# Performance work log

Hardware: AMD Instinct MI355X
Metric: run time of the kernel (lower is better)

## Reference

```python
import jax, jax.numpy as jnp
import numpy as np

B, T, EMB, H1, H2, NL, LMAX, VOCAB = 32, 20, 32, 64, 128, 4, 1024, 85
EPS = 1e-5

def _lengths():
    # ragged per-structure atom counts, max = 1024 (fixes pad length), sum = 24832
    return 1024 - np.arange(B) * 16

def _lstm(x, Wih0, Whh0, b0, WihS, WhhS, bS):
    """NL-layer batch-first LSTM, torch gate order (i,f,g,o), initial h/c = ones
    (matching the torch code's ones init states). Returns stacked final
    (h, c) per layer, each (NL, batch, hidden)."""
    n = x.shape[0]
    hidden = Whh0.shape[1]
    h_fin, c_fin = [], []
    inp = x
    for l in range(NL):
        Wih = Wih0 if l == 0 else WihS[l - 1]
        Whh = Whh0 if l == 0 else WhhS[l - 1]
        bb = b0 if l == 0 else bS[l - 1]
        xg = jnp.einsum('bti,gi->btg', inp, Wih) + bb  # (n, t, 4*hidden)
        init = (jnp.ones((n, hidden), x.dtype), jnp.ones((n, hidden), x.dtype))
        def step(carry, xt, Whh=Whh):
            h, c = carry
            g = xt + h @ Whh.T
            i, f, gg, o = jnp.split(g, 4, axis=-1)
            c = jax.nn.sigmoid(f) * c + jax.nn.sigmoid(i) * jnp.tanh(gg)
            h = jax.nn.sigmoid(o) * jnp.tanh(c)
            return (h, c), h
        (hT, cT), hs = jax.lax.scan(step, init, jnp.swapaxes(xg, 0, 1))
        inp = jnp.swapaxes(hs, 0, 1)
        h_fin.append(hT)
        c_fin.append(cT)
    return jnp.stack(h_fin), jnp.stack(c_fin)

def _bn_rows(x, g, b):
    # BatchNorm1d(batch_size) applied to x.T in torch: per-row (per-structure)
    # normalization over the feature axis, training-mode (biased var).
    m = x.mean(1, keepdims=True)
    v = x.var(1, keepdims=True)
    return (x - m) * jax.lax.rsqrt(v + EPS) * g[:, None] + b[:, None]

def setup_inputs():
    lengths = _lengths()
    N = int(lengths.sum())
    ks = jax.random.split(jax.random.key(0), 32)
    ki = iter(range(32))
    def nrm(shape, s):
        return s * jax.random.normal(ks[next(ki)], shape, jnp.float32)
    return {
        'neighbor_atom_batch': jax.random.randint(ks[next(ki)], (N * T,), 0, VOCAB, dtype=jnp.int32),
        'neighbors_distan_batch': jax.random.normal(ks[next(ki)], (N * T,), jnp.float32),
        'structure_num_bacth': jnp.asarray(lengths, jnp.int32),
        'batch_idx': jnp.asarray(np.repeat(np.arange(B), lengths), jnp.int32),
        'pos_idx': jnp.asarray(np.concatenate([np.arange(l) for l in lengths]), jnp.int32),
        'embed_w': nrm((VOCAB, EMB), 0.02),
        'l1_Wih0': nrm((4 * H1, EMB), 0.05), 'l1_Whh0': nrm((4 * H1, H1), 0.05), 'l1_b0': nrm((4 * H1,), 0.02),
        'l1_Wih': nrm((NL - 1, 4 * H1, H1), 0.05), 'l1_Whh': nrm((NL - 1, 4 * H1, H1), 0.05), 'l1_b': nrm((NL - 1, 4 * H1), 0.02),
        'l2_Wih0': nrm((4 * H2, H1), 0.05), 'l2_Whh0': nrm((4 * H2, H2), 0.05), 'l2_b0': nrm((4 * H2,), 0.02),
        'l2_Wih': nrm((NL - 1, 4 * H2, H2), 0.05), 'l2_Whh': nrm((NL - 1, 4 * H2, H2), 0.05), 'l2_b': nrm((NL - 1, 4 * H2), 0.02),
        'bn2_g': jnp.ones((B,), jnp.float32), 'bn2_b': jnp.zeros((B,), jnp.float32),
        'bn3_g': jnp.ones((B,), jnp.float32), 'bn3_b': jnp.zeros((B,), jnp.float32),
        'w1': nrm((128, 128), 0.1), 'b1': 0.1 * jnp.ones((128,), jnp.float32),
        'w2': nrm((64, 128), 0.1), 'b2': 0.1 * jnp.ones((64,), jnp.float32),
        'w22': nrm((64, 64), 0.1), 'b22': 0.1 * jnp.ones((64,), jnp.float32),
        'w3': nrm((32, 64), 0.1), 'b3': 0.1 * jnp.ones((32,), jnp.float32),
        'w4': nrm((32, 32), 0.1), 'b4': 0.1 * jnp.ones((32,), jnp.float32),
        'w5': nrm((16, 32), 0.1), 'b5': 0.1 * jnp.ones((16,), jnp.float32),
    }

def reference(neighbor_atom_batch, neighbors_distan_batch, structure_num_bacth,
              batch_idx, pos_idx, embed_w,
              l1_Wih0, l1_Whh0, l1_b0, l1_Wih, l1_Whh, l1_b,
              l2_Wih0, l2_Whh0, l2_b0, l2_Wih, l2_Whh, l2_b,
              bn2_g, bn2_b, bn3_g, bn3_b,
              w1, b1, w2, b2, w22, b22, w3, b3, w4, b4, w5, b5):
    # NOTE: neighbors_distan_batch is an argument of the torch forward but is
    # never used by its body; we keep it for signature fidelity.
    # embed, then scale each embedding row by its own integer atom id (as torch does)
    x = embed_w[neighbor_atom_batch] * neighbor_atom_batch.astype(jnp.float32)[:, None]
    x = x.reshape(-1, T, EMB)                       # (N, 20, 32)
    hT, cT = _lstm(x, l1_Wih0, l1_Whh0, l1_b0, l1_Wih, l1_Whh, l1_b)
    d = hT.mean(0) + cT.mean(0)                     # (N, 64)
    # ragged split by structure_num_bacth + pad_sequence -> (B, LMAX, 64), zero padded
    padded = jnp.zeros((B, LMAX, H1), d.dtype).at[batch_idx, pos_idx].set(d)
    # BatchNorm1d(batch_size): channel dim is the structure index -> stats over (len, feat)
    m = padded.mean((1, 2), keepdims=True)
    v = padded.var((1, 2), keepdims=True)
    padded = (padded - m) * jax.lax.rsqrt(v + EPS) * bn2_g[:, None, None] + bn2_b[:, None, None]
    _, cT2 = _lstm(padded, l2_Wih0, l2_Whh0, l2_b0, l2_Wih, l2_Whh, l2_b)
    d = cT2.mean(0)                                 # (B, 128) mean of final cell states
    d = _bn_rows(d, bn3_g, bn3_b)
    d = jax.nn.relu(d @ w1.T + b1)
    d = jax.nn.relu(d @ w2.T + b2)
    d = _bn_rows(d, bn3_g, bn3_b)                   # same BN layer reused, as in torch
    d = jax.nn.relu(d @ w22.T + b22)
    d = jax.nn.relu(d @ w3.T + b3)
    d = jax.nn.relu(d @ w4.T + b4)
    d = d @ w5.T + b5                               # (B, 16)
    return jax.nn.relu(d.sum(1))                    # (B,)
```

## Files before the change

kernel.cpp:

```cpp
#include <hip/hip_runtime.h>


typedef _Float16 f16x8  __attribute__((ext_vector_type(8)));
typedef float    f32x4  __attribute__((ext_vector_type(4)));

#define DEVI static __device__ __forceinline__

constexpr int   T1c   = 20;
constexpr int   EMBc  = 32;
constexpr int   H1c   = 64;
constexpr int   LMAXc = 1024;
constexpr int   VOCABc= 85;
constexpr int   Ntot  = 24832;
constexpr int   NTc   = Ntot * T1c;
constexpr int   R2c   = 32 * LMAXc;
constexpr float EPSc  = 1e-5f;

DEVI float sigm(float x)   { return 1.f / (1.f + __expf(-x)); }
DEVI float tanhf_(float x) { return 1.f - 2.f / (1.f + __expf(2.f * x)); }

DEVI void barrier_lds() {
    asm volatile("s_waitcnt lgkmcnt(0)\n\ts_barrier" ::: "memory");
}
DEVI void drain_vmem() {
    asm volatile("s_waitcnt vmcnt(0)" ::: "memory");
}

__global__ void __launch_bounds__(256)
k_prepw1(const float* __restrict__ Wih0, const float* __restrict__ Whh0,
         const float* __restrict__ WihS, const float* __restrict__ WhhS,
         _Float16* __restrict__ out)
{
    int i = blockIdx.x * 256 + threadIdx.x;
    if (i >= 4 * 256 * 128) return;
    int l = i >> 15, rem = i & 32767, r = rem >> 7, k = rem & 127;
    float v;
    if (l == 0) {
        if (k < 32)      v = Wih0[r * 32 + k];
        else if (k < 64) v = 0.f;
        else             v = Whh0[r * 64 + (k - 64)];
    } else {
        if (k < 64)      v = WihS[((l - 1) * 256 + r) * 64 + k];
        else             v = WhhS[((l - 1) * 256 + r) * 64 + (k - 64)];
    }
    out[i] = (_Float16)v;
}

__global__ void __launch_bounds__(256)
k_prepw2(const float* __restrict__ Wih0, const float* __restrict__ WihS,
         const float* __restrict__ Whh0, const float* __restrict__ WhhS,
         _Float16* __restrict__ wih, _Float16* __restrict__ whh,
         int* __restrict__ flags)
{
    int i = blockIdx.x * 256 + threadIdx.x;
    if (i < 512) flags[i] = (i < 256) ? 0 : 0x7fffffff;
    if (i >= 2 * 4 * 512 * 128) return;
    int half = i >> 18, rem = i & 262143;
    int l = rem >> 16, r = (rem >> 7) & 511, k = rem & 127;
    if (half == 0) {
        float v = (l == 0) ? ((k < 64) ? Wih0[r * 64 + k] : 0.f)
                           : WihS[((l - 1) * 512 + r) * 128 + k];
        wih[rem] = (_Float16)v;
    } else {
        float v = (l == 0) ? Whh0[r * 128 + k]
                           : WhhS[((l - 1) * 512 + r) * 128 + k];
        whh[rem] = (_Float16)v;
    }
}

__global__ void __launch_bounds__(256)
k_scan1all(const int* __restrict__ atoms, const float* __restrict__ ew,
           const _Float16* __restrict__ W16all,
           const float* __restrict__ b0, const float* __restrict__ bS,
           _Float16* __restrict__ seq, float* __restrict__ dacc)
{
    constexpr int SX = 136;
    __shared__ alignas(16) _Float16 xh[32 * SX];
    __shared__ float ewl[VOCABc * EMBc];
    __shared__ int   aidl[32 * T1c];

    const int tid  = threadIdx.x;
    const int lane = tid & 63;
    const int wv   = tid >> 6;
    const int l16  = lane & 15;
    const int quad = lane >> 4;
    const int n0   = blockIdx.x * 32;
    const int d    = wv * 16 + l16;

    for (int i = tid; i < VOCABc * EMBc; i += 256) ewl[i] = ew[i];
    for (int i = tid; i < 32 * T1c; i += 256) aidl[i] = atoms[n0 * T1c + i];

    float daccv[2][4];
#pragma unroll
    for (int mt = 0; mt < 2; ++mt)
#pragma unroll
        for (int r = 0; r < 4; ++r) daccv[mt][r] = 0.f;

    __syncthreads();

#pragma unroll 1
    for (int l = 0; l < 4; ++l) {
        const _Float16* W16  = W16all + (size_t)l * 256 * 128;
        const float*    bptr = (l == 0) ? b0 : bS + (l - 1) * 256;

        float bias[4];
#pragma unroll
        for (int g = 0; g < 4; ++g) bias[g] = bptr[g * 64 + d];

        f16x8 wF[4][4];
#pragma unroll
        for (int kc = 0; kc < 4; ++kc) {
            const int kb = kc * 32 + quad * 8;
#pragma unroll
            for (int g = 0; g < 4; ++g)
                wF[kc][g] = *(const f16x8*)&W16[(size_t)(g * 64 + d) * 128 + kb];
        }

        f32x4 c[2];
        c[0] = {1.f, 1.f, 1.f, 1.f};
        c[1] = {1.f, 1.f, 1.f, 1.f};

        drain_vmem();
        __syncthreads();

#pragma unroll
        for (int mt = 0; mt < 2; ++mt)
#pragma unroll
            for (int r = 0; r < 4; ++r)
                xh[(mt * 16 + quad * 4 + r) * SX + 64 + d] = (_Float16)1.0f;
        if (l == 0)
            for (int idx = tid; idx < 32 * 32; idx += 256) {
                int s = idx >> 5, e = idx & 31;
                xh[s * SX + 32 + e] = (_Float16)0.f;
            }

#pragma unroll 1
        for (int t = 0; t < T1c; ++t) {
            if (l == 0) {
                for (int idx = tid; idx < 32 * 32; idx += 256) {
                    int s = idx >> 5, e = idx & 31;
                    int id = aidl[s * T1c + t];
                    xh[s * SX + e] = (_Float16)(ewl[id * EMBc + e] * (float)id);
                }
            } else {
                for (int idx = tid; idx < 32 * 8; idx += 256) {
                    int s = idx >> 3, k8 = idx & 7;
                    *(f16x8*)&xh[s * SX + k8 * 8] =
                        *(const f16x8*)&seq[((size_t)(n0 + s) * T1c + t) * H1c + k8 * 8];
                }
            }
            __syncthreads();

            f32x4 acc[2][4];
#pragma unroll
            for (int mt = 0; mt < 2; ++mt)
#pragma unroll
                for (int g = 0; g < 4; ++g)
                    acc[mt][g] = {bias[g], bias[g], bias[g], bias[g]};

#pragma unroll
            for (int kc = 0; kc < 4; ++kc) {
                const int kb = kc * 32 + quad * 8;
                f16x8 ah[2];
#pragma unroll
                for (int mt = 0; mt < 2; ++mt)
                    ah[mt] = *(const f16x8*)&xh[(mt * 16 + l16) * SX + kb];
#pragma unroll
                for (int g = 0; g < 4; ++g)
#pragma unroll
                    for (int mt = 0; mt < 2; ++mt)
                        acc[mt][g] = __builtin_amdgcn_mfma_f32_16x16x32_f16(ah[mt], wF[kc][g], acc[mt][g], 0, 0, 0);
            }
            __syncthreads();

#pragma unroll
            for (int mt = 0; mt < 2; ++mt)
#pragma unroll
                for (int r = 0; r < 4; ++r) {
                    float iv = sigm(acc[mt][0][r]);
                    float fv = sigm(acc[mt][1][r]);
                    float gv = tanhf_(acc[mt][2][r]);
                    float ov = sigm(acc[mt][3][r]);
                    float cv = fv * c[mt][r] + iv * gv;
                    c[mt][r] = cv;
                    float hv = ov * tanhf_(cv);
                    _Float16 hf = (_Float16)hv;
                    int s = mt * 16 + quad * 4 + r;
                    xh[s * SX + 64 + d] = hf;
                    if (l < 3)
                        seq[((size_t)(n0 + s) * T1c + t) * H1c + d] = hf;
                    if (t == T1c - 1)
                        daccv[mt][r] += 0.25f * (hv + cv);
                }
        }
    }
#pragma unroll
    for (int mt = 0; mt < 2; ++mt)
#pragma unroll
        for (int r = 0; r < 4; ++r) {
            int s = mt * 16 + quad * 4 + r;
            dacc[(size_t)(n0 + s) * H1c + d] = daccv[mt][r];
        }
}

__global__ void __launch_bounds__(256)
k_bn2_stats(const int* __restrict__ lens, const float* __restrict__ dacc,
            float* __restrict__ stats)
{
    int b = blockIdx.x;
    int off = 0;
    for (int i = 0; i < b; ++i) off += lens[i];
    int len = lens[b];
    const float* base = dacc + (long)off * H1c;
    float s = 0.f, ss = 0.f;
    int total = len * H1c;
    for (int i = threadIdx.x; i < total; i += 256) { float v = base[i]; s += v; ss += v * v; }
    __shared__ float rs[256], rss[256];
    rs[threadIdx.x] = s; rss[threadIdx.x] = ss;
    __syncthreads();
    for (int st = 128; st > 0; st >>= 1) {
        if (threadIdx.x < st) { rs[threadIdx.x] += rs[threadIdx.x + st]; rss[threadIdx.x] += rss[threadIdx.x + st]; }
        __syncthreads();
    }
    if (threadIdx.x == 0) {
        float m = rs[0] / (float)(LMAXc * H1c);
        float v = rss[0] / (float)(LMAXc * H1c) - m * m;
        stats[b]      = m;
        stats[32 + b] = rsqrtf(fmaxf(v, 0.f) + EPSc);
        stats[64 + b] = (float)off;
    }
}

__global__ void __launch_bounds__(256)
k_bn2_apply(const float* __restrict__ dacc, const float* __restrict__ stats,
            const int* __restrict__ lens, const float* __restrict__ g,
            const float* __restrict__ bb, _Float16* __restrict__ outA)
{
    int i = blockIdx.x * 256 + threadIdx.x;
    if (i >= R2c * 128) return;
    int rr = i >> 7, k = i & 127;
    int b = rr >> 10, p = rr & 1023;
    float y = 0.f;
    if (k < H1c) {
        int off = (int)stats[64 + b];
        float x = (p < lens[b]) ? dacc[(off + p) * H1c + k] : 0.f;
        y = (x - stats[b]) * stats[32 + b] * g[b] + bb[b];
    }
    outA[(size_t)(p * 32 + b) * 128 + k] = (_Float16)y;
}

DEVI float qsel(f32x4 a, int quad) {
    float t01 = (quad & 1) ? a[1] : a[0];
    float t23 = (quad & 1) ? a[3] : a[2];
    return (quad & 2) ? t23 : t01;
}

DEVI void spin_ge(const int* fl, int lane, int need)
{
    for (;;) {
        int f = 0x7fffffff;
        if (lane < 8)
            asm volatile("global_load_dword %0, %1, off sc0 sc1\n\ts_waitcnt vmcnt(0)"
                         : "+v"(f) : "v"(fl) : "memory");
        if (__all(f >= need)) break;
    }
}

#define STEP(T, PAR, R, F)                                                          \
  {                                                                                 \
    f32x4 accX[4], accH[4];                                                         \
    _Pragma("unroll") for (int g4 = 0; g4 < 4; ++g4) {                              \
        accX[g4] = {bia[g4], bia[g4], bia[g4], bia[g4]};                            \
        accH[g4] = {0.f, 0.f, 0.f, 0.f};                                            \
    }                                                                               \
    _Pragma("unroll") for (int kc = 0; kc < 4; ++kc) {                              \
        f16x8 ax = *(const f16x8*)&xp[PAR][(l16 & 3) * SH + kc * 32 + quad * 8];    \
        _Pragma("unroll") for (int g4 = 0; g4 < 4; ++g4)                            \
            accX[g4] = __builtin_amdgcn_mfma_f32_16x16x32_f16(ax, wI[g4][kc], accX[g4], 0, 0, 0); \
    }                                                                               \
    _Pragma("unroll") for (int kc = 0; kc < 4; ++kc) {                              \
        f16x8 ah = *(const f16x8*)&av[PAR][(l16 & 3) * SH + kc * 32 + quad * 8];    \
        _Pragma("unroll") for (int g4 = 0; g4 < 4; ++g4)                            \
            accH[g4] = __builtin_amdgcn_mfma_f32_16x16x32_f16(ah, wH[g4][kc], accH[g4], 0, 0, 0); \
    }                                                                               \
    asm volatile("s_waitcnt vmcnt(4)" ::: "memory");                                \
    __builtin_amdgcn_sched_barrier(0);                                              \
    if (lane == 0) {                                                                \
        int fv = (T) - 1;                                                           \
        asm volatile("global_store_dword %0, %1, off sc0 sc1"                       \
                     :: "v"(myflag), "v"(fv) : "memory");                           \
    }                                                                               \
    *(unsigned*)&xp[PAR ^ 1][csam * SH + 2 * coff] = R;                             \
    float gi = qsel(accX[0], quad) + qsel(accH[0], quad);                           \
    float gf = qsel(accX[1], quad) + qsel(accH[1], quad);                           \
    float gg = qsel(accX[2], quad) + qsel(accH[2], quad);                           \
    float go = qsel(accX[3], quad) + qsel(accH[3], quad);                           \
    float cv = sigm(gf) * cst + sigm(gi) * tanhf_(gg);                              \
    cst = cv;                                                                       \
    float hv = sigm(go) * tanhf_(cv);                                               \
    _Float16 hf = (_Float16)hv;                                                     \
    av[PAR ^ 1][quad * SH + cell] = hf;                                             \
    {                                                                               \
        int need = ((T) <= LMAXc - 4) ? (T) + 4 : 0;                                \
        if (!__all(lane >= 8 || F >= need)) spin_ge(sflag, lane, need);             \
    }                                                                               \
    if (l == 0)                                                                     \
        asm volatile("global_load_dword %0, %1, off" : "=v"(R) : "v"(xq) : "memory"); \
    else                                                                            \
        asm volatile("global_load_dword %0, %1, off sc0 sc1" : "=v"(R) : "v"(xq) : "memory"); \
    if ((T) < LMAXc - 4) xq += xstep;                                               \
    {   unsigned hb = (unsigned)__builtin_bit_cast(unsigned short, hf);             \
        asm volatile("global_store_short %0, %1, off sc0 sc1"                       \
                     :: "v"(hp), "v"(hb) : "memory"); }                             \
    hp += 512;                                                                      \
    if (lane < 8)                                                                   \
        asm volatile("global_load_dword %0, %1, off sc0 sc1"                        \
                     : "+v"(F) : "v"(sflag) : "memory");                            \
    barrier_lds();                                                                  \
  }

__global__ void
__attribute__((amdgpu_flat_work_group_size(512, 512), amdgpu_waves_per_eu(2, 2)))
k_scan2p(const _Float16* __restrict__ seqA,
         const _Float16* __restrict__ wihAll,
         const _Float16* __restrict__ whhAll,
         const float* __restrict__ b0,
         const float* __restrict__ bS,
         _Float16* __restrict__ hbuf,
         int* __restrict__ flags,
         float* __restrict__ c2)
{
    constexpr int SH = 144;
    __shared__ alignas(16) _Float16 av[2][4 * SH];
    __shared__ alignas(16) _Float16 xp[2][4 * SH];

    const int bx   = blockIdx.x;
    const int l    = bx & 3;
    const int g    = bx >> 2;
    const int tid  = threadIdx.x;
    const int lane = tid & 63;
    const int w    = tid >> 6;
    const int l16  = lane & 15;
    const int quad = lane >> 4;
    const int cell = w * 16 + l16;

    const _Float16* Wih = wihAll + (size_t)l * 512 * 128;
    const _Float16* Whh = whhAll + (size_t)l * 512 * 128;
    const float*   bptr = (l == 0) ? b0 : bS + (l - 1) * 512;

    f16x8 wI[4][4], wH[4][4];
    float bia[4];
#pragma unroll
    for (int g4 = 0; g4 < 4; ++g4) {
#pragma unroll
        for (int kc = 0; kc < 4; ++kc) {
            const _Float16* pI = &Wih[(size_t)(g4 * 128 + cell) * 128 + kc * 32 + quad * 8];
            const _Float16* pH = &Whh[(size_t)(g4 * 128 + cell) * 128 + kc * 32 + quad * 8];
            asm volatile("global_load_dwordx4 %0, %1, off" : "=v"(wI[g4][kc]) : "v"(pI));
            asm volatile("global_load_dwordx4 %0, %1, off" : "=v"(wH[g4][kc]) : "v"(pH));
        }
        const float* pb = &bptr[g4 * 128 + cell];
        asm volatile("global_load_dword %0, %1, off" : "=v"(bia[g4]) : "v"(pb));
    }
    drain_vmem();
    __builtin_amdgcn_sched_barrier(0);

    const int ci   = tid & 255;
    const int csam = ci >> 6;
    const int coff = ci & 63;

    const unsigned* xq;
    int xstep;
    if (l == 0) {
        xq    = (const unsigned*)seqA + ((size_t)(g * 4 + csam)) * 64 + coff;
        xstep = 32 * 64;
    } else {
        xq    = (const unsigned*)(hbuf + ((size_t)((l - 1) * 8 + g)) * (LMAXc * 512)) + ci;
        xstep = 256;
    }

    _Float16*  hp     = hbuf + ((size_t)(l * 8 + g)) * (LMAXc * 512) + quad * 128 + cell;
    int*       myflag = flags + (l * 8 + g) * 8 + w;
    const int* sflag  = (l == 0) ? (flags + 256 + (lane & 7))
                                 : (flags + ((l - 1) * 8 + g) * 8 + (lane & 7));

    { int s = tid >> 7, e = tid & 127; av[0][s * SH + e] = (_Float16)1.0f; }
    float cst = 1.f;

    unsigned rA, rB;
    int fpreA = 0, fpreB = 0;

    spin_ge(sflag, lane, 1);
    if (l == 0) asm volatile("global_load_dword %0, %1, off" : "=v"(rA) : "v"(xq) : "memory");
    else        asm volatile("global_load_dword %0, %1, off sc0 sc1" : "=v"(rA) : "v"(xq) : "memory");
    drain_vmem();
    __builtin_amdgcn_sched_barrier(0);
    *(unsigned*)&xp[0][csam * SH + 2 * coff] = rA;

    spin_ge(sflag, lane, 2);
    {
        const unsigned* p1 = xq + xstep;
        if (l == 0) asm volatile("global_load_dword %0, %1, off" : "=v"(rA) : "v"(p1) : "memory");
        else        asm volatile("global_load_dword %0, %1, off sc0 sc1" : "=v"(rA) : "v"(p1) : "memory");
    }
    drain_vmem();
    __builtin_amdgcn_sched_barrier(0);

    spin_ge(sflag, lane, 3);
    {
        const unsigned* p2 = xq + 2 * xstep;
        if (l == 0) asm volatile("global_load_dword %0, %1, off" : "=v"(rB) : "v"(p2) : "memory");
        else        asm volatile("global_load_dword %0, %1, off sc0 sc1" : "=v"(rB) : "v"(p2) : "memory");
    }
    if (lane < 8) {
        asm volatile("global_load_dword %0, %1, off sc0 sc1" : "+v"(fpreA) : "v"(sflag) : "memory");
        asm volatile("global_load_dword %0, %1, off sc0 sc1" : "+v"(fpreB) : "v"(sflag) : "memory");
    }
    xq += 3 * (size_t)xstep;
    __syncthreads();

#pragma unroll 1
    for (int t = 0; t < LMAXc; t += 2) {
        STEP(t,     0, rA, fpreA)
        STEP(t + 1, 1, rB, fpreB)
    }

    drain_vmem();
    if (lane == 0) {
        int fin = LMAXc;
        asm volatile("global_store_dword %0, %1, off sc0 sc1"
                     :: "v"(myflag), "v"(fin) : "memory");
    }
    c2[(size_t)l * 4096 + (g * 4 + quad) * 128 + cell] = 0.25f * cst;
}

DEVI void bn_rows_dev(float* X, int K, const float* g, const float* bb,
                      float* mv, int tid)
{
    __syncthreads();
    if (tid < 32) {
        float s = 0.f, ss = 0.f;
        const float* r = X + tid * K;
        for (int k = 0; k < K; ++k) { float v = r[k]; s += v; ss += v * v; }
        float m = s / (float)K;
        float vv = ss / (float)K - m * m;
        mv[tid]      = m;
        mv[32 + tid] = rsqrtf(fmaxf(vv, 0.f) + EPSc);
    }
    __syncthreads();
    for (int i = tid; i < 32 * K; i += 256) {
        int b = i / K;
        X[i] = (X[i] - mv[b]) * mv[32 + b] * g[b] + bb[b];
    }
    __syncthreads();
}

DEVI void lin_dev(const float* X, int K, const float* W, const float* bias,
                  int NO, float* Y, int relu, int tid)
{
    __syncthreads();
    for (int i = tid; i < 32 * NO; i += 256) {
        int b = i / NO, j = i - b * NO;
        float a = bias[j];
        const float* xr = X + b * K;
        const float* wr = W + j * K;
        for (int k = 0; k < K; ++k) a += xr[k] * wr[k];
        Y[i] = relu ? fmaxf(a, 0.f) : a;
    }
    __syncthreads();
}

__global__ void __launch_bounds__(256)
k_head(const float* __restrict__ c2, const float* __restrict__ g3, const float* __restrict__ bb3,
       const float* w1, const float* b1, const float* w2, const float* b2,
       const float* w22, const float* b22, const float* w3, const float* b3,
       const float* w4, const float* b4, const float* w5, const float* b5,
       float* __restrict__ out)
{
    __shared__ float A[32 * 128];
    __shared__ float Bf[32 * 128];
    __shared__ float mv[64];
    const int tid = threadIdx.x;

    for (int i = tid; i < 32 * 128; i += 256)
        A[i] = c2[i] + c2[4096 + i] + c2[8192 + i] + c2[12288 + i];
    bn_rows_dev(A, 128, g3, bb3, mv, tid);
    lin_dev(A, 128, w1, b1, 128, Bf, 1, tid);
    lin_dev(Bf, 128, w2, b2, 64, A, 1, tid);
    bn_rows_dev(A, 64, g3, bb3, mv, tid);
    lin_dev(A, 64, w22, b22, 64, Bf, 1, tid);
    lin_dev(Bf, 64, w3, b3, 32, A, 1, tid);
    lin_dev(A, 32, w4, b4, 32, Bf, 1, tid);
    lin_dev(Bf, 32, w5, b5, 16, A, 0, tid);
    if (tid < 32) {
        float s = 0.f;
        for (int j = 0; j < 16; ++j) s += A[tid * 16 + j];
        out[tid] = fmaxf(s, 0.f);
    }
}

extern "C" void kernel_launch(void* const* d_in, const int* in_sizes, int n_in,
                              void* d_out, int out_size, void* d_ws, size_t ws_size,
                              hipStream_t stream)
{
    const int*   atoms  = (const int*)d_in[0];
    const int*   lens   = (const int*)d_in[2];
    const float* embw   = (const float*)d_in[5];
    const float* l1Wih0 = (const float*)d_in[6];
    const float* l1Whh0 = (const float*)d_in[7];
    const float* l1b0   = (const float*)d_in[8];
    const float* l1Wih  = (const float*)d_in[9];
    const float* l1Whh  = (const float*)d_in[10];
    const float* l1b    = (const float*)d_in[11];
    const float* l2Wih0 = (const float*)d_in[12];
    const float* l2Whh0 = (const float*)d_in[13];
    const float* l2b0   = (const float*)d_in[14];
    const float* l2Wih  = (const float*)d_in[15];
    const float* l2Whh  = (const float*)d_in[16];
    const float* l2b    = (const float*)d_in[17];
    const float* bn2g   = (const float*)d_in[18];
    const float* bn2b   = (const float*)d_in[19];
    const float* bn3g   = (const float*)d_in[20];
    const float* bn3b   = (const float*)d_in[21];
    const float* w1  = (const float*)d_in[22]; const float* b1  = (const float*)d_in[23];
    const float* w2  = (const float*)d_in[24]; const float* b2  = (const float*)d_in[25];
    const float* w22 = (const float*)d_in[26]; const float* b22 = (const float*)d_in[27];
    const float* w3  = (const float*)d_in[28]; const float* b3  = (const float*)d_in[29];
    const float* w4  = (const float*)d_in[30]; const float* b4  = (const float*)d_in[31];
    const float* w5  = (const float*)d_in[32]; const float* b5  = (const float*)d_in[33];
    float* out = (float*)d_out;

    char* base = (char*)d_ws;
    size_t off = 0;
    auto take = [&](size_t bytes) -> char* {
        char* p = base + off;
        off = (off + bytes + 255) & ~(size_t)255;
        return p;
    };
    _Float16* seq1f  = (_Float16*)take((size_t)NTc * H1c * 2);
    float*    dacc   = (float*)take((size_t)Ntot * H1c * 4);
    _Float16* wcomb1 = (_Float16*)take((size_t)4 * 256 * 128 * 2);
    _Float16* wih16  = (_Float16*)take((size_t)4 * 512 * 128 * 2);
    _Float16* whh16  = (_Float16*)take((size_t)4 * 512 * 128 * 2);
    _Float16* seqA   = (_Float16*)take((size_t)R2c * 128 * 2);
    _Float16* hbuf   = (_Float16*)take((size_t)4 * 8 * LMAXc * 512 * 2);
    int*      flags  = (int*)take(512 * sizeof(int));
    float*    stats  = (float*)take(1024);
    float*    c2     = (float*)take((size_t)4 * 32 * 128 * 4);

    k_prepw1<<<(4 * 256 * 128 + 255) / 256, 256, 0, stream>>>(l1Wih0, l1Whh0, l1Wih, l1Whh, wcomb1);
    k_prepw2<<<(2 * 4 * 512 * 128 + 255) / 256, 256, 0, stream>>>(l2Wih0, l2Wih, l2Whh0, l2Whh, wih16, whh16, flags);

    k_scan1all<<<Ntot / 32, 256, 0, stream>>>(atoms, embw, wcomb1, l1b0, l1b, seq1f, dacc);

    k_bn2_stats<<<32, 256, 0, stream>>>(lens, dacc, stats);
    k_bn2_apply<<<(R2c * 128 + 255) / 256, 256, 0, stream>>>(dacc, stats, lens, bn2g, bn2b, seqA);

    k_scan2p<<<32, 512, 0, stream>>>(seqA, wih16, whh16, l2b0, l2b, hbuf, flags, c2);

    k_head<<<1, 256, 0, stream>>>(c2, bn3g, bn3b, w1, b1, w2, b2, w22, b22,
                                  w3, b3, w4, b4, w5, b5, out);

    (void)in_sizes; (void)n_in; (void)out_size; (void)ws_size;
}
```

Measured before the change: 1.746 ms.

## Split LSTM2 into recurrent and input-projection workgroups with a ring buffer

The second LSTM scan kernel now launches twice as many workgroups. Half compute only the recurrent h·Whh product per step. The other half precompute the input projection x·Wih plus bias four timesteps at a time and hand the gate pre-activations over through a 64-slot ring buffer in global memory, synchronised with flags. Weights move from registers into LDS. The aim is to shorten the serial per-step critical path by taking the input GEMM off it, at the cost of extra global traffic, spin-waits on flags, and more complex cross-block synchronisation.

Result: slower. 2.743 ms (+57.2%).

```diff
diff --git a/kernel.cpp b/kernel.cpp
--- a/kernel.cpp
+++ b/kernel.cpp
@@ -2,9 +2,11 @@
 
 
 typedef _Float16 f16x8  __attribute__((ext_vector_type(8)));
+typedef _Float16 f16x4  __attribute__((ext_vector_type(4)));
 typedef float    f32x4  __attribute__((ext_vector_type(4)));
 
 #define DEVI static __device__ __forceinline__
+#define MF(a, b, c) __builtin_amdgcn_mfma_f32_16x16x32_f16(a, b, c, 0, 0, 0)
 
 constexpr int   T1c   = 20;
 constexpr int   EMBc  = 32;
@@ -15,6 +17,7 @@
 constexpr int   NTc   = Ntot * T1c;
 constexpr int   R2c   = 32 * LMAXc;
 constexpr float EPSc  = 1e-5f;
+constexpr int   SH    = 144;
 
 DEVI float sigm(float x)   { return 1.f / (1.f + __expf(-x)); }
 DEVI float tanhf_(float x) { return 1.f - 2.f / (1.f + __expf(2.f * x)); }
@@ -53,7 +56,7 @@
          int* __restrict__ flags)
 {
     int i = blockIdx.x * 256 + threadIdx.x;
-    if (i < 512) flags[i] = (i < 256) ? 0 : 0x7fffffff;
+    if (i < 768) flags[i] = (i < 512) ? 0 : 0x7fffffff;
     if (i >= 2 * 4 * 512 * 128) return;
     int half = i >> 18, rem = i & 262143;
     int l = rem >> 16, r = (rem >> 7) & 511, k = rem & 127;
@@ -169,7 +172,7 @@
                 for (int g = 0; g < 4; ++g)
 #pragma unroll
                     for (int mt = 0; mt < 2; ++mt)
-                        acc[mt][g] = __builtin_amdgcn_mfma_f32_16x16x32_f16(ah[mt], wF[kc][g], acc[mt][g], 0, 0, 0);
+                        acc[mt][g] = MF(ah[mt], wF[kc][g], acc[mt][g]);
             }
             __syncthreads();
 
@@ -266,49 +269,42 @@
     }
 }
 
-#define STEP(T, PAR, R, F)                                                          \
+#define STEPH(T, PAR, RU, F)                                                        \
   {                                                                                 \
-    f32x4 accX[4], accH[4];                                                         \
-    _Pragma("unroll") for (int g4 = 0; g4 < 4; ++g4) {                              \
-        accX[g4] = {bia[g4], bia[g4], bia[g4], bia[g4]};                            \
-        accH[g4] = {0.f, 0.f, 0.f, 0.f};                                            \
-    }                                                                               \
-    _Pragma("unroll") for (int kc = 0; kc < 4; ++kc) {                              \
-        f16x8 ax = *(const f16x8*)&xp[PAR][(l16 & 3) * SH + kc * 32 + quad * 8];    \
-        _Pragma("unroll") for (int g4 = 0; g4 < 4; ++g4)                            \
-            accX[g4] = __builtin_amdgcn_mfma_f32_16x16x32_f16(ax, wI[g4][kc], accX[g4], 0, 0, 0); \
-    }                                                                               \
+    f32x4 a0 = {0,0,0,0}, a1 = {0,0,0,0}, a2 = {0,0,0,0}, a3 = {0,0,0,0};           \
     _Pragma("unroll") for (int kc = 0; kc < 4; ++kc) {                              \
         f16x8 ah = *(const f16x8*)&av[PAR][(l16 & 3) * SH + kc * 32 + quad * 8];    \
-        _Pragma("unroll") for (int g4 = 0; g4 < 4; ++g4)                            \
-            accH[g4] = __builtin_amdgcn_mfma_f32_16x16x32_f16(ah, wH[g4][kc], accH[g4], 0, 0, 0); \
-    }                                                                               \
-    asm volatile("s_waitcnt vmcnt(4)" ::: "memory");                                \
+        a0 = MF(ah, *(const f16x8*)&wL[(0 * 4 + kc) * 4096 + wbase], a0);           \
+        a1 = MF(ah, *(const f16x8*)&wL[(1 * 4 + kc) * 4096 + wbase], a1);           \
+        a2 = MF(ah, *(const f16x8*)&wL[(2 * 4 + kc) * 4096 + wbase], a2);           \
+        a3 = MF(ah, *(const f16x8*)&wL[(3 * 4 + kc) * 4096 + wbase], a3);           \
+    }                                                                               \
+    asm volatile("s_waitcnt vmcnt(28)" ::: "memory");                               \
     __builtin_amdgcn_sched_barrier(0);                                              \
     if (lane == 0) {                                                                \
-        int fv = (T) - 1;                                                           \
+        int fv = (T) >= 7 ? (T) - 7 : 0;                                            \
         asm volatile("global_store_dword %0, %1, off sc0 sc1"                       \
                      :: "v"(myflag), "v"(fv) : "memory");                           \
     }                                                                               \
-    *(unsigned*)&xp[PAR ^ 1][csam * SH + 2 * coff] = R;                             \
-    float gi = qsel(accX[0], quad) + qsel(accH[0], quad);                           \
-    float gf = qsel(accX[1], quad) + qsel(accH[1], quad);                           \
-    float gg = qsel(accX[2], quad) + qsel(accH[2], quad);                           \
-    float go = qsel(accX[3], quad) + qsel(accH[3], quad);                           \
+    float gi = qsel(a0, quad) + (float)RU[0];                                       \
+    float gf = qsel(a1, quad) + (float)RU[1];                                       \
+    float gg = qsel(a2, quad) + (float)RU[2];                                       \
+    float go = qsel(a3, quad) + (float)RU[3];                                       \
     float cv = sigm(gf) * cst + sigm(gi) * tanhf_(gg);                              \
     cst = cv;                                                                       \
     float hv = sigm(go) * tanhf_(cv);                                               \
     _Float16 hf = (_Float16)hv;                                                     \
     av[PAR ^ 1][quad * SH + cell] = hf;                                             \
     {                                                                               \
-        int need = ((T) <= LMAXc - 4) ? (T) + 4 : 0;                                \
+        int need = ((T) + 9 <= LMAXc) ? (T) + 9 : LMAXc;                            \
         if (!__all(lane >= 8 || F >= need)) spin_ge(sflag, lane, need);             \
     }                                                                               \
-    if (l == 0)                                                                     \
-        asm volatile("global_load_dword %0, %1, off" : "=v"(R) : "v"(xq) : "memory"); \
-    else                                                                            \
-        asm volatile("global_load_dword %0, %1, off sc0 sc1" : "=v"(R) : "v"(xq) : "memory"); \
-    if ((T) < LMAXc - 4) xq += xstep;                                               \
+    {                                                                               \
+        int tu = (T) + 8; if (tu > LMAXc - 1) tu = LMAXc - 1;                       \
+        const _Float16* up = ubase + (size_t)(((tu & 63) * 4 + quad) * 128 + cell) * 4; \
+        asm volatile("global_load_dwordx2 %0, %1, off sc0 sc1"                      \
+                     : "=v"(RU) : "v"(up) : "memory");                              \
+    }                                                                               \
     {   unsigned hb = (unsigned)__builtin_bit_cast(unsigned short, hf);             \
         asm volatile("global_store_short %0, %1, off sc0 sc1"                       \
                      :: "v"(hp), "v"(hb) : "memory"); }                             \
@@ -319,6 +315,67 @@
     barrier_lds();                                                                  \
   }
 
+#define XLOADW(R, P)                                                                \
+    if (l == 0) asm volatile("global_load_dword %0, %1, off" : "=v"(R) : "v"(P) : "memory"); \
+    else        asm volatile("global_load_dword %0, %1, off sc0 sc1" : "=v"(R) : "v"(P) : "memory");
+
+#define ITERW(J, PARX, RA, RB, FA, FT)                                              \
+  {                                                                                 \
+    f32x4 bb = *(const f32x4*)&bL2[cell * 4];                                       \
+    f32x4 a0 = {bb[0],bb[0],bb[0],bb[0]}, a1 = {bb[1],bb[1],bb[1],bb[1]};           \
+    f32x4 a2 = {bb[2],bb[2],bb[2],bb[2]}, a3 = {bb[3],bb[3],bb[3],bb[3]};           \
+    _Pragma("unroll") for (int kc = 0; kc < 4; ++kc) {                              \
+        f16x8 ax = *(const f16x8*)&xp4[PARX][l16 * SH + kc * 32 + quad * 8];        \
+        a0 = MF(ax, *(const f16x8*)&wL[(0 * 4 + kc) * 4096 + wbase], a0);           \
+        a1 = MF(ax, *(const f16x8*)&wL[(1 * 4 + kc) * 4096 + wbase], a1);           \
+        a2 = MF(ax, *(const f16x8*)&wL[(2 * 4 + kc) * 4096 + wbase], a2);           \
+        a3 = MF(ax, *(const f16x8*)&wL[(3 * 4 + kc) * 4096 + wbase], a3);           \
+    }                                                                               \
+    asm volatile("s_waitcnt vmcnt(27)" ::: "memory");                               \
+    __builtin_amdgcn_sched_barrier(0);                                              \
+    if (lane == 0) {                                                                \
+        int fv = 4 * (J) - 12; if (fv < 0) fv = 0;                                  \
+        asm volatile("global_store_dword %0, %1, off sc0 sc1"                       \
+                     :: "v"(myflag), "v"(fv) : "memory");                           \
+    }                                                                               \
+    *(unsigned*)&xp4[PARX ^ 1][rowA * SH + 2 * dcol] = RA;                          \
+    *(unsigned*)&xp4[PARX ^ 1][rowB * SH + 2 * dcol] = RB;                          \
+    {                                                                               \
+        int nt = 4 * (J) - 52; if (nt < 0) nt = 0;                                  \
+        if (!__all(lane >= 8 || FT >= nt)) spin_ge(sflagT, lane, nt);               \
+    }                                                                               \
+    {                                                                               \
+        int slot = (4 * (J) + quad) & 63;                                           \
+        _Pragma("unroll") for (int r = 0; r < 4; ++r) {                             \
+            f16x4 uv;                                                               \
+            uv[0] = (_Float16)a0[r]; uv[1] = (_Float16)a1[r];                       \
+            uv[2] = (_Float16)a2[r]; uv[3] = (_Float16)a3[r];                       \
+            _Float16* up = ubase + (size_t)((slot * 4 + r) * 128 + cell) * 4;       \
+            asm volatile("global_store_dwordx2 %0, %1, off sc0 sc1"                 \
+                         :: "v"(up), "v"(uv) : "memory");                           \
+        }                                                                           \
+    }                                                                               \
+    {                                                                               \
+        int na = 4 * (J) + 24; if (na > LMAXc) na = LMAXc;                          \
+        if (!__all(lane >= 8 || FA >= na)) spin_ge(sflagA, lane, na);               \
+    }                                                                               \
+    {                                                                               \
+        int ta = 4 * (J) + 20 + jA; if (ta > LMAXc - 1) ta = LMAXc - 1;             \
+        int tb = 4 * (J) + 20 + jB; if (tb > LMAXc - 1) tb = LMAXc - 1;             \
+        const unsigned* pa = xb + (size_t)ta * xstepw + baseA;                      \
+        const unsigned* pb = xb + (size_t)tb * xstepw + baseB;                      \
+        XLOADW(RA, pa)                                                              \
+        XLOADW(RB, pb)                                                              \
+    }                                                                               \
+    if (lane < 8) {                                                                 \
+        asm volatile("global_load_dword %0, %1, off sc0 sc1"                        \
+                     : "+v"(FA) : "v"(sflagA) : "memory");                          \
+        asm volatile("global_load_dword %0, %1, off sc0 sc1"                        \
+                     : "+v"(FT) : "v"(sflagT) : "memory");                          \
+    }                                                                               \
+    barrier_lds();                                                                  \
+  }
+
 __global__ void
 __attribute__((amdgpu_flat_work_group_size(512, 512), amdgpu_waves_per_eu(2, 2)))
 k_scan2p(const _Float16* __restrict__ seqA,
@@ -327,111 +384,165 @@
          const float* __restrict__ b0,
          const float* __restrict__ bS,
          _Float16* __restrict__ hbuf,
+         _Float16* __restrict__ ubuf,
          int* __restrict__ flags,
          float* __restrict__ c2)
 {
-    constexpr int SH = 144;
-    __shared__ alignas(16) _Float16 av[2][4 * SH];
-    __shared__ alignas(16) _Float16 xp[2][4 * SH];
+    __shared__ alignas(16) char smem[131072 + 11776];
+    _Float16* wL = (_Float16*)smem;
 
     const int bx   = blockIdx.x;
-    const int l    = bx & 3;
-    const int g    = bx >> 2;
     const int tid  = threadIdx.x;
     const int lane = tid & 63;
     const int w    = tid >> 6;
     const int l16  = lane & 15;
     const int quad = lane >> 4;
     const int cell = w * 16 + l16;
-
-    const _Float16* Wih = wihAll + (size_t)l * 512 * 128;
-    const _Float16* Whh = whhAll + (size_t)l * 512 * 128;
-    const float*   bptr = (l == 0) ? b0 : bS + (l - 1) * 512;
-
-    f16x8 wI[4][4], wH[4][4];
-    float bia[4];
-#pragma unroll
-    for (int g4 = 0; g4 < 4; ++g4) {
-#pragma unroll
-        for (int kc = 0; kc < 4; ++kc) {
-            const _Float16* pI = &Wih[(size_t)(g4 * 128 + cell) * 128 + kc * 32 + quad * 8];
-            const _Float16* pH = &Whh[(size_t)(g4 * 128 + cell) * 128 + kc * 32 + quad * 8];
-            asm volatile("global_load_dwordx4 %0, %1, off" : "=v"(wI[g4][kc]) : "v"(pI));
-            asm volatile("global_load_dwordx4 %0, %1, off" : "=v"(wH[g4][kc]) : "v"(pH));
-        }
-        const float* pb = &bptr[g4 * 128 + cell];
-        asm volatile("global_load_dword %0, %1, off" : "=v"(bia[g4]) : "v"(pb));
-    }
-    drain_vmem();
-    __builtin_amdgcn_sched_barrier(0);
-
-    const int ci   = tid & 255;
-    const int csam = ci >> 6;
-    const int coff = ci & 63;
-
-    const unsigned* xq;
-    int xstep;
-    if (l == 0) {
-        xq    = (const unsigned*)seqA + ((size_t)(g * 4 + csam)) * 64 + coff;
-        xstep = 32 * 64;
+    const int wbase = (w * 64 + lane) * 8;
+
+    if (bx < 32) {
+        const int l = bx & 3, g = bx >> 2;
+        const _Float16* W = whhAll + (size_t)l * 512 * 128;
+        _Float16* avm = (_Float16*)(smem + 131072);
+        _Float16* const av[2] = { avm, avm + 4 * SH };
+
+        for (int c = tid; c < 8192; c += 512) {
+            int gk = c >> 9, r2 = c & 511;
+            int wv2 = r2 >> 6, ln = r2 & 63;
+            int row = (gk >> 2) * 128 + wv2 * 16 + (ln & 15);
+            *(f16x8*)&wL[(size_t)c * 8] =
+                *(const f16x8*)&W[(size_t)row * 128 + (gk & 3) * 32 + (ln >> 4) * 8];
+        }
+        av[0][quad * SH + cell] = (_Float16)1.0f;
+        float cst = 1.f;
+
+        const _Float16* ubase = ubuf + (size_t)(l * 8 + g) * (64 * 4 * 512);
+        _Float16*  hp     = hbuf + (size_t)(l * 8 + g) * (LMAXc * 512) + quad * 128 + cell;
+        int*       myflag = flags + (l * 8 + g) * 8 + w;
+        const int* sflag  = flags + 256 + (l * 8 + g) * 8 + (lane & 7);
+
+        __syncthreads();
+        spin_ge(sflag, lane, 8);
+        f16x4 rU0, rU1, rU2, rU3, rU4, rU5, rU6, rU7;
+#define ULOADP(R, I)                                                                \
+        { const _Float16* up = ubase + (size_t)(((I) * 4 + quad) * 128 + cell) * 4; \
+          asm volatile("global_load_dwordx2 %0, %1, off sc0 sc1"                    \
+                       : "=v"(R) : "v"(up) : "memory"); }
+        ULOADP(rU0, 0) ULOADP(rU1, 1) ULOADP(rU2, 2) ULOADP(rU3, 3)
+        ULOADP(rU4, 4) ULOADP(rU5, 5) ULOADP(rU6, 6) ULOADP(rU7, 7)
+#undef ULOADP
+        int fpreA = 0, fpreB = 0;
+        if (lane < 8) {
+            asm volatile("global_load_dword %0, %1, off sc0 sc1" : "+v"(fpreA) : "v"(sflag) : "memory");
+            asm volatile("global_load_dword %0, %1, off sc0 sc1" : "+v"(fpreB) : "v"(sflag) : "memory");
+        }
+        drain_vmem();
+        __builtin_amdgcn_sched_barrier(0);
+        __syncthreads();
+
+#pragma unroll 1
+        for (int t = 0; t < LMAXc; t += 8) {
+            STEPH(t + 0, 0, rU0, fpreA)
+            STEPH(t + 1, 1, rU1, fpreB)
+            STEPH(t + 2, 0, rU2, fpreA)
+            STEPH(t + 3, 1, rU3, fpreB)
+            STEPH(t + 4, 0, rU4, fpreA)
+            STEPH(t + 5, 1, rU5, fpreB)
+            STEPH(t + 6, 0, rU6, fpreA)
+            STEPH(t + 7, 1, rU7, fpreB)
+        }
+
+        drain_vmem();
+        if (lane == 0) {
+            int fin = 2048;
+            asm volatile("global_store_dword %0, %1, off sc0 sc1"
+                         :: "v"(myflag), "v"(fin) : "memory");
+        }
+        c2[(size_t)l * 4096 + (g * 4 + quad) * 128 + cell] = 0.25f * cst;
     } else {
-        xq    = (const unsigned*)(hbuf + ((size_t)((l - 1) * 8 + g)) * (LMAXc * 512)) + ci;
-        xstep = 256;
-    }
-
-    _Float16*  hp     = hbuf + ((size_t)(l * 8 + g)) * (LMAXc * 512) + quad * 128 + cell;
-    int*       myflag = flags + (l * 8 + g) * 8 + w;
-    const int* sflag  = (l == 0) ? (flags + 256 + (lane & 7))
-                                 : (flags + ((l - 1) * 8 + g) * 8 + (lane & 7));
-
-    { int s = tid >> 7, e = tid & 127; av[0][s * SH + e] = (_Float16)1.0f; }
-    float cst = 1.f;
-
-    unsigned rA, rB;
-    int fpreA = 0, fpreB = 0;
-
-    spin_ge(sflag, lane, 1);
-    if (l == 0) asm volatile("global_load_dword %0, %1, off" : "=v"(rA) : "v"(xq) : "memory");
-    else        asm volatile("global_load_dword %0, %1, off sc0 sc1" : "=v"(rA) : "v"(xq) : "memory");
-    drain_vmem();
-    __builtin_amdgcn_sched_barrier(0);
-    *(unsigned*)&xp[0][csam * SH + 2 * coff] = rA;
-
-    spin_ge(sflag, lane, 2);
-    {
-        const unsigned* p1 = xq + xstep;
-        if (l == 0) asm volatile("global_load_dword %0, %1, off" : "=v"(rA) : "v"(p1) : "memory");
-        else        asm volatile("global_load_dword %0, %1, off sc0 sc1" : "=v"(rA) : "v"(p1) : "memory");
-    }
-    drain_vmem();
-    __builtin_amdgcn_sched_barrier(0);
-
-    spin_ge(sflag, lane, 3);
-    {
-        const unsigned* p2 = xq + 2 * xstep;
-        if (l == 0) asm volatile("global_load_dword %0, %1, off" : "=v"(rB) : "v"(p2) : "memory");
-        else        asm volatile("global_load_dword %0, %1, off sc0 sc1" : "=v"(rB) : "v"(p2) : "memory");
-    }
-    if (lane < 8) {
-        asm volatile("global_load_dword %0, %1, off sc0 sc1" : "+v"(fpreA) : "v"(sflag) : "memory");
-        asm volatile("global_load_dword %0, %1, off sc0 sc1" : "+v"(fpreB) : "v"(sflag) : "memory");
-    }
-    xq += 3 * (size_t)xstep;
-    __syncthreads();
+        const int l = (bx - 32) & 3, g = (bx - 32) >> 2;
+        const _Float16* W = wihAll + (size_t)l * 512 * 128;
+        const float* bptr = (l == 0) ? b0 : bS + (l - 1) * 512;
+        _Float16* xpm = (_Float16*)(smem + 131072);
+        _Float16* const xp4[2] = { xpm, xpm + 16 * SH };
+        float* bL2 = (float*)(smem + 131072 + 9216);
+
+        for (int c = tid; c < 8192; c += 512) {
+            int gk = c >> 9, r2 = c & 511;
+            int wv2 = r2 >> 6, ln = r2 & 63;
+            int row = (gk >> 2) * 128 + wv2 * 16 + (ln & 15);
+            *(f16x8*)&wL[(size_t)c * 8] =
+                *(const f16x8*)&W[(size_t)row * 128 + (gk & 3) * 32 + (ln >> 4) * 8];
+        }
+        bL2[(tid & 127) * 4 + (tid >> 7)] = bptr[(tid >> 7) * 128 + (tid & 127)];
+
+        _Float16*  ubase  = ubuf + (size_t)(l * 8 + g) * (64 * 4 * 512);
+        int*       myflag = flags + 256 + (l * 8 + g) * 8 + w;
+        const int* sflagA = (l == 0) ? flags + 512 + (lane & 7)
+                                     : flags + ((l - 1) * 8 + g) * 8 + (lane & 7);
+        const int* sflagT = flags + (l * 8 + g) * 8 + (lane & 7);
+
+        const int dcol = tid & 63;
+        const int rowA = tid >> 6, rowB = 8 + rowA;
+        const int sA = rowA & 3, jA = rowA >> 2;
+        const int sB = rowB & 3, jB = rowB >> 2;
+        const unsigned* xb;
+        int xstepw, baseA, baseB;
+        if (l == 0) {
+            xb = (const unsigned*)seqA;
+            xstepw = 2048;
+            baseA = (g * 4 + sA) * 64 + dcol;
+            baseB = (g * 4 + sB) * 64 + dcol;
+        } else {
+            xb = (const unsigned*)(hbuf + (size_t)((l - 1) * 8 + g) * (LMAXc * 512));
+            xstepw = 256;
+            baseA = sA * 64 + dcol;
+            baseB = sB * 64 + dcol;
+        }
+
+        __syncthreads();
+        spin_ge(sflagA, lane, 20);
+        unsigned rxa0, rxb0, rxa1, rxb1, rxa2, rxb2, rxa3, rxb3;
+        {
+            unsigned r0, r1;
+            const unsigned* pa = xb + (size_t)jA * xstepw + baseA;
+            const unsigned* pb = xb + (size_t)jB * xstepw + baseB;
+            XLOADW(r0, pa) XLOADW(r1, pb)
+            drain_vmem();
+            __builtin_amdgcn_sched_barrier(0);
+            *(unsigned*)&xp4[0][rowA * SH + 2 * dcol] = r0;
+            *(unsigned*)&xp4[0][rowB * SH + 2 * dcol] = r1;
+        }
+#define XPRE(RA, RB, P)                                                             \
+        { const unsigned* pa = xb + (size_t)(4 * ((P) + 1) + jA) * xstepw + baseA;  \
+          const unsigned* pb = xb + (size_t)(4 * ((P) + 1) + jB) * xstepw + baseB;  \
+          XLOADW(RA, pa) XLOADW(RB, pb) }
+        XPRE(rxa0, rxb0, 0) XPRE(rxa1, rxb1, 1) XPRE(rxa2, rxb2, 2) XPRE(rxa3, rxb3, 3)
+#undef XPRE
+        int fA = 0, fT = 0;
+        if (lane < 8) {
+            asm volatile("global_load_dword %0, %1, off sc0 sc1" : "+v"(fA) : "v"(sflagA) : "memory");
+            asm volatile("global_load_dword %0, %1, off sc0 sc1" : "+v"(fT) : "v"(sflagT) : "memory");
+        }
+        drain_vmem();
+        __builtin_amdgcn_sched_barrier(0);
+        __syncthreads();
 
 #pragma unroll 1
-    for (int t = 0; t < LMAXc; t += 2) {
-        STEP(t,     0, rA, fpreA)
-        STEP(t + 1, 1, rB, fpreB)
-    }
-
-    drain_vmem();
-    if (lane == 0) {
-        int fin = LMAXc;
-        asm volatile("global_store_dword %0, %1, off sc0 sc1"
-                     :: "v"(myflag), "v"(fin) : "memory");
-    }
-    c2[(size_t)l * 4096 + (g * 4 + quad) * 128 + cell] = 0.25f * cst;
+        for (int j = 0; j < 64; ++j) {
+            ITERW(4 * j + 0, 0, rxa0, rxb0, fA, fT)
+            ITERW(4 * j + 1, 1, rxa1, rxb1, fA, fT)
+            ITERW(4 * j + 2, 0, rxa2, rxb2, fA, fT)
+            ITERW(4 * j + 3, 1, rxa3, rxb3, fA, fT)
+        }
+
+        drain_vmem();
+        if (lane == 0) {
+            int fin = 2048;
+            asm volatile("global_store_dword %0, %1, off sc0 sc1"
+                         :: "v"(myflag), "v"(fin) : "memory");
+        }
+    }
 }
 
 DEVI void bn_rows_dev(float* X, int K, const float* g, const float* bb,
@@ -544,7 +655,8 @@
     _Float16* whh16  = (_Float16*)take((size_t)4 * 512 * 128 * 2);
     _Float16* seqA   = (_Float16*)take((size_t)R2c * 128 * 2);
     _Float16* hbuf   = (_Float16*)take((size_t)4 * 8 * LMAXc * 512 * 2);
-    int*      flags  = (int*)take(512 * sizeof(int));
+    _Float16* ubuf   = (_Float16*)take((size_t)4 * 8 * 64 * 4 * 512 * 2);
+    int*      flags  = (int*)take(768 * sizeof(int));
     float*    stats  = (float*)take(1024);
     float*    c2     = (float*)take((size_t)4 * 32 * 128 * 4);
 
@@ -556,7 +668,7 @@
     k_bn2_stats<<<32, 256, 0, stream>>>(lens, dacc, stats);
     k_bn2_apply<<<(R2c * 128 + 255) / 256, 256, 0, stream>>>(dacc, stats, lens, bn2g, bn2b, seqA);
 
-    k_scan2p<<<32, 512, 0, stream>>>(seqA, wih16, whh16, l2b0, l2b, hbuf, flags, c2);
+    k_scan2p<<<64, 512, 0, stream>>>(seqA, wih16, whh16, l2b0, l2b, hbuf, ubuf, flags, c2);
 
     k_head<<<1, 256, 0, stream>>>(c2, bn3g, bn3b, w1, b1, w2, b2, w22, b22,
                                   w3, b3, w4, b4, w5, b5, out);
```

## Keep layer-1 LSTM inter-layer sequence in LDS instead of global memory

Applied to the files above, without the earlier changes.

The first LSTM stack now keeps each layer's hidden-state sequence for a 32-atom tile in shared memory, so the next layer reads it from LDS rather than writing it to and re-reading it from a global workspace. The single combined input/hidden tile becomes a separate embedding tile plus a double-buffered hidden-state tile, which drops one of the barriers around the recurrent state. The goal is to remove global memory traffic and load latency on the recurrence critical path. The cost is about 120 KB of LDS per block, which sharply limits how many blocks can sit on a CU at once and reduces latency hiding for this latency-bound recurrent kernel.

Result: slower. 1.833 ms (+5.0%).

```diff
diff --git a/kernel.cpp b/kernel.cpp
--- a/kernel.cpp
+++ b/kernel.cpp
@@ -5,6 +5,7 @@
 typedef float    f32x4  __attribute__((ext_vector_type(4)));
 
 #define DEVI static __device__ __forceinline__
+#define MF(a, b, c) __builtin_amdgcn_mfma_f32_16x16x32_f16(a, b, c, 0, 0, 0)
 
 constexpr int   T1c   = 20;
 constexpr int   EMBc  = 32;
@@ -12,7 +13,6 @@
 constexpr int   LMAXc = 1024;
 constexpr int   VOCABc= 85;
 constexpr int   Ntot  = 24832;
-constexpr int   NTc   = Ntot * T1c;
 constexpr int   R2c   = 32 * LMAXc;
 constexpr float EPSc  = 1e-5f;
 
@@ -72,10 +72,11 @@
 k_scan1all(const int* __restrict__ atoms, const float* __restrict__ ew,
            const _Float16* __restrict__ W16all,
            const float* __restrict__ b0, const float* __restrict__ bS,
-           _Float16* __restrict__ seq, float* __restrict__ dacc)
-{
-    constexpr int SX = 136;
-    __shared__ alignas(16) _Float16 xh[32 * SX];
+           float* __restrict__ dacc)
+{
+    __shared__ alignas(16) _Float16 seqL[T1c * 32 * 72];
+    __shared__ alignas(16) _Float16 xe[32 * 72];
+    __shared__ alignas(16) _Float16 hP[2][32 * 72];
     __shared__ float ewl[VOCABc * EMBc];
     __shared__ int   aidl[32 * T1c];
 
@@ -89,6 +90,7 @@
 
     for (int i = tid; i < VOCABc * EMBc; i += 256) ewl[i] = ew[i];
     for (int i = tid; i < 32 * T1c; i += 256) aidl[i] = atoms[n0 * T1c + i];
+    for (int i = tid; i < 32 * 72; i += 256) xe[i] = (_Float16)0.f;
 
     float daccv[2][4];
 #pragma unroll
@@ -120,19 +122,16 @@
         c[0] = {1.f, 1.f, 1.f, 1.f};
         c[1] = {1.f, 1.f, 1.f, 1.f};
 
-        drain_vmem();
         __syncthreads();
 
 #pragma unroll
         for (int mt = 0; mt < 2; ++mt)
 #pragma unroll
             for (int r = 0; r < 4; ++r)
-                xh[(mt * 16 + quad * 4 + r) * SX + 64 + d] = (_Float16)1.0f;
-        if (l == 0)
-            for (int idx = tid; idx < 32 * 32; idx += 256) {
-                int s = idx >> 5, e = idx & 31;
-                xh[s * SX + 32 + e] = (_Float16)0.f;
-            }
+                hP[0][(mt * 16 + quad * 4 + r) * 72 + d] = (_Float16)1.0f;
+
+        int par = 0;
+        __syncthreads();
 
 #pragma unroll 1
         for (int t = 0; t < T1c; ++t) {
@@ -140,13 +139,7 @@
                 for (int idx = tid; idx < 32 * 32; idx += 256) {
                     int s = idx >> 5, e = idx & 31;
                     int id = aidl[s * T1c + t];
-                    xh[s * SX + e] = (_Float16)(ewl[id * EMBc + e] * (float)id);
-                }
-            } else {
-                for (int idx = tid; idx < 32 * 8; idx += 256) {
-                    int s = idx >> 3, k8 = idx & 7;
-                    *(f16x8*)&xh[s * SX + k8 * 8] =
-                        *(const f16x8*)&seq[((size_t)(n0 + s) * T1c + t) * H1c + k8 * 8];
+                    xe[s * 72 + e] = (_Float16)(ewl[id * EMBc + e] * (float)id);
                 }
             }
             __syncthreads();
@@ -160,16 +153,24 @@
 
 #pragma unroll
             for (int kc = 0; kc < 4; ++kc) {
-                const int kb = kc * 32 + quad * 8;
                 f16x8 ah[2];
 #pragma unroll
-                for (int mt = 0; mt < 2; ++mt)
-                    ah[mt] = *(const f16x8*)&xh[(mt * 16 + l16) * SX + kb];
+                for (int mt = 0; mt < 2; ++mt) {
+                    const int row = mt * 16 + l16;
+                    const _Float16* src;
+                    if (kc < 2)
+                        src = (l == 0)
+                            ? &xe[row * 72 + kc * 32 + quad * 8]
+                            : &seqL[(t * 32 + row) * 72 + kc * 32 + quad * 8];
+                    else
+                        src = &hP[par][row * 72 + (kc - 2) * 32 + quad * 8];
+                    ah[mt] = *(const f16x8*)src;
+                }
 #pragma unroll
                 for (int g = 0; g < 4; ++g)
 #pragma unroll
                     for (int mt = 0; mt < 2; ++mt)
-                        acc[mt][g] = __builtin_amdgcn_mfma_f32_16x16x32_f16(ah[mt], wF[kc][g], acc[mt][g], 0, 0, 0);
+                        acc[mt][g] = MF(ah[mt], wF[kc][g], acc[mt][g]);
             }
             __syncthreads();
 
@@ -186,12 +187,13 @@
                     float hv = ov * tanhf_(cv);
                     _Float16 hf = (_Float16)hv;
                     int s = mt * 16 + quad * 4 + r;
-                    xh[s * SX + 64 + d] = hf;
+                    hP[par ^ 1][s * 72 + d] = hf;
                     if (l < 3)
-                        seq[((size_t)(n0 + s) * T1c + t) * H1c + d] = hf;
+                        seqL[(t * 32 + s) * 72 + d] = hf;
                     if (t == T1c - 1)
                         daccv[mt][r] += 0.25f * (hv + cv);
                 }
+            par ^= 1;
         }
     }
 #pragma unroll
@@ -276,12 +278,12 @@
     _Pragma("unroll") for (int kc = 0; kc < 4; ++kc) {                              \
         f16x8 ax = *(const f16x8*)&xp[PAR][(l16 & 3) * SH + kc * 32 + quad * 8];    \
         _Pragma("unroll") for (int g4 = 0; g4 < 4; ++g4)                            \
-            accX[g4] = __builtin_amdgcn_mfma_f32_16x16x32_f16(ax, wI[g4][kc], accX[g4], 0, 0, 0); \
+            accX[g4] = MF(ax, wI[g4][kc], accX[g4]);                                \
     }                                                                               \
     _Pragma("unroll") for (int kc = 0; kc < 4; ++kc) {                              \
         f16x8 ah = *(const f16x8*)&av[PAR][(l16 & 3) * SH + kc * 32 + quad * 8];    \
         _Pragma("unroll") for (int g4 = 0; g4 < 4; ++g4)                            \
-            accH[g4] = __builtin_amdgcn_mfma_f32_16x16x32_f16(ah, wH[g4][kc], accH[g4], 0, 0, 0); \
+            accH[g4] = MF(ah, wH[g4][kc], accH[g4]);                                \
     }                                                                               \
     asm volatile("s_waitcnt vmcnt(4)" ::: "memory");                                \
     __builtin_amdgcn_sched_barrier(0);                                              \
@@ -537,7 +539,6 @@
         off = (off + bytes + 255) & ~(size_t)255;
         return p;
     };
-    _Float16* seq1f  = (_Float16*)take((size_t)NTc * H1c * 2);
     float*    dacc   = (float*)take((size_t)Ntot * H1c * 4);
     _Float16* wcomb1 = (_Float16*)take((size_t)4 * 256 * 128 * 2);
     _Float16* wih16  = (_Float16*)take((size_t)4 * 512 * 128 * 2);
@@ -551,7 +552,7 @@
     k_prepw1<<<(4 * 256 * 128 + 255) / 256, 256, 0, stream>>>(l1Wih0, l1Whh0, l1Wih, l1Whh, wcomb1);
     k_prepw2<<<(2 * 4 * 512 * 128 + 255) / 256, 256, 0, stream>>>(l2Wih0, l2Wih, l2Whh0, l2Whh, wih16, whh16, flags);
 
-    k_scan1all<<<Ntot / 32, 256, 0, stream>>>(atoms, embw, wcomb1, l1b0, l1b, seq1f, dacc);
+    k_scan1all<<<Ntot / 32, 256, 0, stream>>>(atoms, embw, wcomb1, l1b0, l1b, dacc);
 
     k_bn2_stats<<<32, 256, 0, stream>>>(lens, dacc, stats);
     k_bn2_apply<<<(R2c * 128 + 255) / 256, 256, 0, stream>>>(dacc, stats, lens, bn2g, bn2b, seqA);
```
